# Kernel optimization log

Hardware: AMD Instinct MI355X
Metric: run time of the kernel (lower is better)

Reference implementation:

```python
import jax, jax.numpy as jnp
import numpy as np

NEG = -1000000.0  # mask value used by the torch module


def setup_inputs() -> dict:
    key = jax.random.key(0)
    kq, kk, kv, kl = jax.random.split(key, 4)
    B, Lq, Lk, d = 16, 2048, 2048, 128
    queries = jax.random.normal(kq, (B, Lq, d), dtype=jnp.float32)
    keys = jax.random.normal(kk, (B, Lk, d), dtype=jnp.float32)
    values = jax.random.normal(kv, (B, Lk, d), dtype=jnp.float32)
    valid_lens = jax.random.randint(kl, (B,), 1, Lk + 1, dtype=jnp.int64)
    return {"queries": queries, "keys": keys, "values": values, "valid_lens": valid_lens}


def reference(queries, keys, values, valid_lens):
    d = queries.shape[-1]
    # scores: [B, Lq, Lk]
    scores = jnp.einsum("bqd,bkd->bqk", queries, keys) / jnp.sqrt(jnp.asarray(d, queries.dtype))
    # valid_lens is [B]; mask key positions >= valid_len (broadcast over query rows)
    Lk = keys.shape[1]
    mask = jnp.arange(Lk)[None, None, :] < valid_lens[:, None, None]  # [B, 1, Lk]
    scores = jnp.where(mask, scores, NEG)
    attn = jax.nn.softmax(scores, axis=-1)
    # dropout p=0.0 -> identity
    return jnp.einsum("bqk,bkd->bqd", attn, values)
```

## Files before the change

kernel.cpp:

```cpp
#include <hip/hip_runtime.h>
#include <hip/hip_fp16.h>


typedef _Float16 f16x2 __attribute__((ext_vector_type(2)));
typedef _Float16 f16x8 __attribute__((ext_vector_type(8)));
typedef __fp16   n16x2 __attribute__((ext_vector_type(2)));
typedef float    f32x4 __attribute__((ext_vector_type(4)));
typedef float    f32x16 __attribute__((ext_vector_type(16)));
typedef unsigned int  u32;
typedef unsigned int  u32x4 __attribute__((ext_vector_type(4)));

#define LQ 2048
#define LK 2048
#define DIM 128
#define TILEB 16384
#define HTILEB 8192
#define BATCHB (32 * TILEB)
#define CFIX 10.0f

__device__ __forceinline__ f16x2 cvt2(float a, float b) {
    n16x2 t = __builtin_amdgcn_cvt_pkrtz(a, b);
    return __builtin_bit_cast(f16x2, t);
}
__device__ __forceinline__ u32 cvt2u(float a, float b) {
    return __builtin_bit_cast(u32, __builtin_amdgcn_cvt_pkrtz(a, b));
}

__device__ __forceinline__ f16x8 pk8(float4 a, float4 b) {
    f16x2 p0 = cvt2(a.x, a.y), p1 = cvt2(a.z, a.w);
    f16x2 p2 = cvt2(b.x, b.y), p3 = cvt2(b.z, b.w);
    f16x8 r;
    r[0]=p0[0]; r[1]=p0[1]; r[2]=p1[0]; r[3]=p1[1];
    r[4]=p2[0]; r[5]=p2[1]; r[6]=p3[0]; r[7]=p3[1];
    return r;
}

__global__ __launch_bounds__(256)
void prepK_kernel(const float* __restrict__ K, char* __restrict__ Kf,
                  const int* __restrict__ VLg) {
    size_t e = ((size_t)blockIdx.x * 256 + threadIdx.x) * 8;
    size_t krow = e >> 7; int d0 = (int)(e & 127);
    size_t b = krow >> 11; int k = (int)(krow & 2047);
    if (k >= VLg[b]) return;
    float4 a = *(const float4*)(K + e);
    float4 c = *(const float4*)(K + e + 4);
    int t = k >> 6, g = (k >> 5) & 1, lo = k & 31;
    int u = d0 >> 3, dc = u >> 1, hi = u & 1;
    char* out = Kf + ((b * 32 + t) * 16 + g * 8 + dc) * 1024 + (hi * 32 + lo) * 16;
    *(f16x8*)out = pk8(a, c);
}

__global__ __launch_bounds__(256)
void prepV_kernel(const float* __restrict__ V, char* __restrict__ Vf,
                  const int* __restrict__ VLg) {
    __shared__ _Float16 tl[64 * 136];
    const int blk = blockIdx.x, tid = threadIdx.x;
    const int b = blk >> 5, t = blk & 31, k0g = t * 64;
    if (k0g >= VLg[b]) return;
    const float* src = V + ((size_t)b * LK + k0g) * DIM;
    #pragma unroll
    for (int i = 0; i < 4; ++i) {
        int e = i * 2048 + tid * 8;
        int row = e >> 7, d = e & 127;
        float4 a = *(const float4*)(src + row * DIM + d);
        float4 c = *(const float4*)(src + row * DIM + d + 4);
        *(f16x8*)(&tl[row * 136 + d]) = pk8(a, c);
    }
    __syncthreads();
    char* out = Vf + (size_t)(b * 32 + t) * TILEB;
    #pragma unroll
    for (int c = 0; c < 4; ++c) {
        int chunk = tid * 4 + c;
        int f2 = chunk >> 6, l = chunk & 63;
        int ks = f2 >> 2, dc2 = f2 & 3;
        int k0 = ks * 16 + (l >> 5) * 8;
        int d  = dc2 * 32 + (l & 31);
        f16x8 w;
        #pragma unroll
        for (int j = 0; j < 8; ++j) w[j] = tl[(k0 + j) * 136 + d];
        *(f16x8*)(out + f2 * 1024 + l * 16) = w;
    }
}

__global__ __launch_bounds__(256, 2)
void fa_kernel(const float* __restrict__ Qg, const char* __restrict__ Kf,
               const char* __restrict__ Vf, const int* __restrict__ VLg,
               float* __restrict__ Og)
{
    __shared__ float scr_o[2][32 * 128];
    __shared__ float scr_l[2][32];

    const int tid = threadIdx.x, wv = tid >> 6, lane = tid & 63;
    const int lo = lane & 31, hi = lane >> 5;
    const int qh = wv & 1, kh = wv >> 1;
    const int blk = blockIdx.x;

    unsigned long long ord = 0;
    {
        int vl[16];
        #pragma unroll
        for (int i = 0; i < 16; ++i) vl[i] = VLg[i];
        unsigned used = 0;
        #pragma unroll
        for (int r = 0; r < 16; ++r) {
            int best = 0, bl = -1;
            #pragma unroll
            for (int i = 0; i < 16; ++i)
                if (!((used >> i) & 1) && vl[i] > bl) { bl = vl[i]; best = i; }
            used |= 1u << best;
            ord |= (unsigned long long)best << (4 * r);
        }
    }
    const int half = blk >> 8, slot = blk & 15, j = (blk >> 4) & 15;
    const int rank = half ? (15 - slot) : slot;
    const int b    = (int)((ord >> (4 * rank)) & 15);
    const int qt   = half ? (16 + j) : j;
    const int q0   = qt * 64 + qh * 32;

    const int nvalid = VLg[b];
    const int H = (nvalid + 31) >> 5;
    const float SCL = 0.08838834764831845f * 1.44269504088896341f;

    const char* Kfb = Kf + (size_t)b * BATCHB + lane * 16;
    const char* Vfb = Vf + (size_t)b * BATCHB + lane * 16;

    f16x8 qf[8];
    {
        const float* qr = Qg + ((size_t)b*LQ + q0 + lo)*DIM + hi*8;
        #pragma unroll
        for (int dc = 0; dc < 8; ++dc) {
            float4 a = *(const float4*)(qr + dc*16);
            float4 c = *(const float4*)(qr + dc*16 + 4);
            a.x*=SCL; a.y*=SCL; a.z*=SCL; a.w*=SCL;
            c.x*=SCL; c.y*=SCL; c.z*=SCL; c.w*=SCL;
            qf[dc] = pk8(a, c);
        }
    }

    f32x16 oacc[4];
    #pragma unroll
    for (int d = 0; d < 4; ++d)
        #pragma unroll
        for (int r = 0; r < 16; ++r) oacc[d][r] = 0.f;
    float lrow = 0.f;

    f16x8 kA[8], kB[8], vC[8];

    auto load_k = [&](f16x8* kf, int h) {
        const char* kp = Kfb + (size_t)h * HTILEB;
        #pragma unroll
        for (int f = 0; f < 8; ++f) kf[f] = *(const f16x8*)(kp + f * 1024);
    };
    auto load_v = [&](int h) {
        const char* vp = Vfb + (size_t)h * HTILEB;
        #pragma unroll
        for (int f = 0; f < 8; ++f) vC[f] = *(const f16x8*)(vp + f * 1024);
    };

    auto compute = [&](const f16x8* kf, int h) {
        f32x16 s;
        #pragma unroll
        for (int r = 0; r < 16; ++r) s[r] = 0.f;
        __builtin_amdgcn_s_setprio(1);
        #pragma unroll
        for (int dc = 0; dc < 8; ++dc)
            s = __builtin_amdgcn_mfma_f32_32x32x16_f16(kf[dc], qf[dc], s, 0, 0, 0);
        __builtin_amdgcn_s_setprio(0);

        if ((h + 1) * 32 > nvalid) {
            const int k0 = h * 32;
            #pragma unroll
            for (int r = 0; r < 16; ++r) {
                int key = k0 + (r & 3) + 8 * (r >> 2) + 4 * hi;
                if (key >= nvalid) s[r] = -1e30f;
            }
        }

        u32 c[8];
        float rs = 0.f;
        #pragma unroll
        for (int m = 0; m < 8; ++m) {
            float a0 = __builtin_amdgcn_exp2f(s[2*m]   - CFIX);
            float a1 = __builtin_amdgcn_exp2f(s[2*m+1] - CFIX);
            rs += a0 + a1;
            c[m] = cvt2u(a0, a1);
        }
        lrow += rs;

        u32 w[8];
        #pragma unroll
        for (int m = 0; m < 8; ++m) w[m] = __shfl_xor(c[m], 32);
        f16x8 pa0 = __builtin_bit_cast(f16x8, hi ? (u32x4){w[2],w[3],c[2],c[3]}
                                                 : (u32x4){c[0],c[1],w[0],w[1]});
        f16x8 pa1 = __builtin_bit_cast(f16x8, hi ? (u32x4){w[6],w[7],c[6],c[7]}
                                                 : (u32x4){c[4],c[5],w[4],w[5]});

        __builtin_amdgcn_s_setprio(1);
        #pragma unroll
        for (int dc2 = 0; dc2 < 4; ++dc2) {
            oacc[dc2] = __builtin_amdgcn_mfma_f32_32x32x16_f16(pa0, vC[    dc2], oacc[dc2], 0,0,0);
            oacc[dc2] = __builtin_amdgcn_mfma_f32_32x32x16_f16(pa1, vC[4 + dc2], oacc[dc2], 0,0,0);
        }
        __builtin_amdgcn_s_setprio(0);
    };

    int h = kh;
    if (h < H) load_k(kA, h);
    while (h < H) {
        const int h2 = h + 2, h4 = h + 4;
        load_v(h);
        if (h2 < H) load_k(kB, h2);
        compute(kA, h);
        if (h2 < H) {
            load_v(h2);
            if (h4 < H) load_k(kA, h4);
            compute(kB, h2);
        }
        h = h4;
    }

    lrow += __shfl_xor(lrow, 32);

    if (kh == 1) {
        float* so = &scr_o[qh][0];
        #pragma unroll
        for (int r = 0; r < 16; ++r) {
            int qr = (r & 3) + 8 * (r >> 2) + 4 * hi;
            #pragma unroll
            for (int dc2 = 0; dc2 < 4; ++dc2)
                so[qr * 128 + dc2 * 32 + lo] = oacc[dc2][r];
        }
        if (hi == 0) scr_l[qh][lo] = lrow;
    }
    __syncthreads();
    if (kh == 0) {
        const float* so = &scr_o[qh][0];
        float lt = lrow + scr_l[qh][lo];
        float linv = 1.f / lt;
        #pragma unroll
        for (int r = 0; r < 16; ++r) {
            int qr = (r & 3) + 8 * (r >> 2) + 4 * hi;
            float lv = __shfl(linv, qr);
            float* orow = Og + ((size_t)b*LQ + q0 + qr)*DIM + lo;
            #pragma unroll
            for (int dc2 = 0; dc2 < 4; ++dc2)
                orow[dc2*32] = (oacc[dc2][r] + so[qr * 128 + dc2 * 32 + lo]) * lv;
        }
    }
}

typedef _Float16 f16x4_t __attribute__((ext_vector_type(4)));
__device__ __forceinline__ float fel(const float4& a, const float4& b, int d) {
    const float arr[8] = {a.x,a.y,a.z,a.w,b.x,b.y,b.z,b.w};
    return arr[d];
}
__device__ __forceinline__ int kfo(int r, int dbyte) {
    return ((r << 8) + dbyte) ^ ((r & 7) << 4);
}
__device__ __forceinline__ int vto(int d, int k) {
    return d*128 + ((((k >> 3) ^ ((d ^ (d >> 3)) & 7)) << 4) + (k & 7) * 2);
}

__global__ __launch_bounds__(256, 2)
void fa_fb(const float* __restrict__ Qg, const float* __restrict__ Kg,
           const float* __restrict__ Vg, const int* __restrict__ VLg,
           float* __restrict__ Og)
{
    __shared__ __align__(16) char ldsbuf[2][32768];
    __shared__ __align__(16) char ldsP[4][2048];
    const int tid = threadIdx.x, wv = tid >> 6, lane = tid & 63;
    const int lg = lane >> 4, ln = lane & 15;
    const int blk = blockIdx.x;
    const int b = 2 * (blk & 7) + ((blk >> 3) & 1);
    const int q0 = (blk >> 4) * 64 + wv * 16;
    const int nvalid = VLg[b];
    const int nt = (nvalid + 63) >> 6;
    const float SCL = 0.08838834764831845f * 1.44269504088896341f;
    const float* Kb32 = Kg + (size_t)b * LK * DIM;
    const float* Vb32 = Vg + (size_t)b * LK * DIM;
    float4 ka[4], kb4[4], va[4], vb[4];
    auto issue = [&](int t) {
        int k0 = t * 64;
        #pragma unroll
        for (int i = 0; i < 4; ++i) {
            int c = tid + i*256, row = c >> 4, d0 = (c & 15) * 8;
            const float* s = Kb32 + (size_t)(k0 + row)*DIM + d0;
            ka[i] = *(const float4*)s;  kb4[i] = *(const float4*)(s+4);
        }
        int kq = tid >> 4, d0 = (tid & 15) * 8;
        #pragma unroll
        for (int j = 0; j < 4; ++j) {
            const float* s = Vb32 + (size_t)(k0 + kq*4 + j)*DIM + d0;
            va[j] = *(const float4*)s;  vb[j] = *(const float4*)(s+4);
        }
    };
    auto swr = [&](int buf) {
        char* kb = &ldsbuf[buf][0];
        char* vb2 = &ldsbuf[buf][16384];
        #pragma unroll
        for (int i = 0; i < 4; ++i) {
            int c = tid + i*256, row = c >> 4, d0 = (c & 15) * 8;
            *(f16x8*)(kb + kfo(row, d0 << 1)) = pk8(ka[i], kb4[i]);
        }
        int kq = tid >> 4, d0 = (tid & 15) * 8;
        #pragma unroll
        for (int dd = 0; dd < 8; ++dd) {
            f16x2 lw = cvt2(fel(va[0],vb[0],dd), fel(va[1],vb[1],dd));
            f16x2 hw = cvt2(fel(va[2],vb[2],dd), fel(va[3],vb[3],dd));
            f16x4_t w; w[0]=lw[0]; w[1]=lw[1]; w[2]=hw[0]; w[3]=hw[1];
            *(f16x4_t*)(vb2 + vto(d0 + dd, 4*kq)) = w;
        }
    };
    issue(0);
    f16x8 qf[4];
    {
        const float* qr = Qg + ((size_t)b*LQ + q0 + ln)*DIM + lg*8;
        #pragma unroll
        for (int dc = 0; dc < 4; ++dc) {
            float4 a = *(const float4*)(qr + dc*32);
            float4 c = *(const float4*)(qr + dc*32 + 4);
            a.x*=SCL; a.y*=SCL; a.z*=SCL; a.w*=SCL;
            c.x*=SCL; c.y*=SCL; c.z*=SCL; c.w*=SCL;
            qf[dc] = pk8(a, c);
        }
    }
    swr(0);
    __syncthreads();
    f32x4 acc[8];
    #pragma unroll
    for (int t = 0; t < 8; ++t) acc[t] = (f32x4){0.f,0.f,0.f,0.f};
    float lrow = 0.f;
    char* pbase = &ldsP[wv][0];
    int cur = 0;
    for (int t = 0; t < nt; ++t) {
        const int k0 = t * 64;
        const bool more = (t + 1 < nt);
        if (more) issue(t + 1);
        char* kbase = &ldsbuf[cur][0];
        char* vbase = &ldsbuf[cur][16384];
        f32x4 s[4];
        #pragma unroll
        for (int kc = 0; kc < 4; ++kc) s[kc] = (f32x4){0.f,0.f,0.f,0.f};
        #pragma unroll
        for (int kc = 0; kc < 4; ++kc)
            #pragma unroll
            for (int dc = 0; dc < 4; ++dc) {
                f16x8 kf = *(const f16x8*)(kbase + kfo(kc*16 + ln, dc*64 + lg*16));
                s[kc] = __builtin_amdgcn_mfma_f32_16x16x32_f16(kf, qf[dc], s[kc], 0,0,0);
            }
        if (k0 + 64 > nvalid) {
            #pragma unroll
            for (int kc = 0; kc < 4; ++kc)
                #pragma unroll
                for (int r = 0; r < 4; ++r)
                    if (k0 + kc*16 + 4*lg + r >= nvalid) s[kc][r] = -1e30f;
        }
        float rs = 0.f;
        #pragma unroll
        for (int kc = 0; kc < 4; ++kc) {
            float p0 = __builtin_amdgcn_exp2f(s[kc][0] - CFIX);
            float p1 = __builtin_amdgcn_exp2f(s[kc][1] - CFIX);
            float p2 = __builtin_amdgcn_exp2f(s[kc][2] - CFIX);
            float p3 = __builtin_amdgcn_exp2f(s[kc][3] - CFIX);
            rs += (p0 + p1) + (p2 + p3);
            f16x2 plo = cvt2(p0, p1);
            f16x2 phi = cvt2(p2, p3);
            f16x4_t w; w[0]=plo[0]; w[1]=plo[1]; w[2]=phi[0]; w[3]=phi[1];
            *(f16x4_t*)(pbase + (ln << 7) + ((kc*32 + lg*8) ^ ((ln & 7) << 4))) = w;
        }
        lrow += rs;
        asm volatile("s_waitcnt lgkmcnt(0)" ::: "memory");
        f16x8 af[2];
        #pragma unroll
        for (int kc2 = 0; kc2 < 2; ++kc2)
            af[kc2] = *(const f16x8*)(pbase + (ln << 7) + ((kc2*64 + lg*16) ^ ((ln & 7) << 4)));
        #pragma unroll
        for (int tt = 0; tt < 8; ++tt)
            #pragma unroll
            for (int kc2 = 0; kc2 < 2; ++kc2) {
                f16x8 bf = *(const f16x8*)(vbase + vto(tt*16 + ln, kc2*32 + lg*8));
                acc[tt] = __builtin_amdgcn_mfma_f32_16x16x32_f16(af[kc2], bf, acc[tt], 0,0,0);
            }
        if (more) { swr(cur ^ 1); __syncthreads(); cur ^= 1; }
    }
    lrow += __shfl_xor(lrow, 16);
    lrow += __shfl_xor(lrow, 32);
    float linv = 1.f / lrow;
    #pragma unroll
    for (int r = 0; r < 4; ++r) {
        float lr = __shfl(linv, 4*lg + r);
        float* orow = Og + ((size_t)b*LQ + q0 + 4*lg + r)*DIM + ln;
        #pragma unroll
        for (int tt = 0; tt < 8; ++tt) orow[tt*16] = acc[tt][r] * lr;
    }
}

extern "C" void kernel_launch(void* const* d_in, const int* in_sizes, int n_in,
                              void* d_out, int out_size, void* d_ws, size_t ws_size,
                              hipStream_t stream) {
    const float* Q  = (const float*)d_in[0];
    const float* K  = (const float*)d_in[1];
    const float* V  = (const float*)d_in[2];
    const int*   VL = (const int*)d_in[3];
    float* O = (float*)d_out;

    const size_t need = (size_t)16 * BATCHB * 2;
    if (ws_size >= need) {
        char* Kf = (char*)d_ws;
        char* Vf = Kf + (size_t)16 * BATCHB;
        prepK_kernel<<<dim3(2048), dim3(256), 0, stream>>>(K, Kf, VL);
        prepV_kernel<<<dim3(512),  dim3(256), 0, stream>>>(V, Vf, VL);
        fa_kernel<<<dim3(512), dim3(256), 0, stream>>>(Q, Kf, Vf, VL, O);
    } else {
        fa_fb<<<dim3(512), dim3(256), 0, stream>>>(Q, K, V, VL, O);
    }
}
```

Measured before the change: 53.83 us.

## Stage K/V tiles through double-buffered LDS via global_load_lds shared across waves

```diff
diff --git a/kernel.cpp b/kernel.cpp
--- a/kernel.cpp
+++ b/kernel.cpp
@@ -87,8 +87,7 @@
                const char* __restrict__ Vf, const int* __restrict__ VLg,
                float* __restrict__ Og)
 {
-    __shared__ float scr_o[2][32 * 128];
-    __shared__ float scr_l[2][32];
+    __shared__ __align__(16) char ldsbuf[2][2][16384];
 
     const int tid = threadIdx.x, wv = tid >> 6, lane = tid & 63;
     const int lo = lane & 31, hi = lane >> 5;
@@ -119,10 +118,11 @@
 
     const int nvalid = VLg[b];
     const int H = (nvalid + 31) >> 5;
+    const int T = (H + 1) >> 1;
     const float SCL = 0.08838834764831845f * 1.44269504088896341f;
 
-    const char* Kfb = Kf + (size_t)b * BATCHB + lane * 16;
-    const char* Vfb = Vf + (size_t)b * BATCHB + lane * 16;
+    const char* Kfb = Kf + (size_t)b * BATCHB;
+    const char* Vfb = Vf + (size_t)b * BATCHB;
 
     f16x8 qf[8];
     {
@@ -144,27 +144,30 @@
         for (int r = 0; r < 16; ++r) oacc[d][r] = 0.f;
     float lrow = 0.f;
 
-    f16x8 kA[8], kB[8], vC[8];
-
-    auto load_k = [&](f16x8* kf, int h) {
-        const char* kp = Kfb + (size_t)h * HTILEB;
-        #pragma unroll
-        for (int f = 0; f < 8; ++f) kf[f] = *(const f16x8*)(kp + f * 1024);
+    auto dma = [&](int bu, int h) {
+        const char* src = (qh ? Vfb : Kfb) + (size_t)h * HTILEB + lane * 16;
+        char* dst = &ldsbuf[kh][bu][qh ? 8192 : 0];
+        #pragma unroll
+        for (int c = 0; c < 8; ++c)
+            __builtin_amdgcn_global_load_lds(
+                (const __attribute__((address_space(1))) unsigned*)(src + c * 1024),
+                (__attribute__((address_space(3))) unsigned*)(dst + c * 1024),
+                16, 0, 0);
     };
-    auto load_v = [&](int h) {
-        const char* vp = Vfb + (size_t)h * HTILEB;
-        #pragma unroll
-        for (int f = 0; f < 8; ++f) vC[f] = *(const f16x8*)(vp + f * 1024);
-    };
-
-    auto compute = [&](const f16x8* kf, int h) {
+
+    auto compute = [&](int cur, int h) {
+        char* ldsK = &ldsbuf[kh][cur][0];
+        char* ldsV = &ldsbuf[kh][cur][8192];
+
         f32x16 s;
         #pragma unroll
         for (int r = 0; r < 16; ++r) s[r] = 0.f;
         __builtin_amdgcn_s_setprio(1);
         #pragma unroll
-        for (int dc = 0; dc < 8; ++dc)
-            s = __builtin_amdgcn_mfma_f32_32x32x16_f16(kf[dc], qf[dc], s, 0, 0, 0);
+        for (int dc = 0; dc < 8; ++dc) {
+            f16x8 kfr = *(const f16x8*)(ldsK + dc * 1024 + lane * 16);
+            s = __builtin_amdgcn_mfma_f32_32x32x16_f16(kfr, qf[dc], s, 0, 0, 0);
+        }
         __builtin_amdgcn_s_setprio(0);
 
         if ((h + 1) * 32 > nvalid) {
@@ -198,44 +201,43 @@
         __builtin_amdgcn_s_setprio(1);
         #pragma unroll
         for (int dc2 = 0; dc2 < 4; ++dc2) {
-            oacc[dc2] = __builtin_amdgcn_mfma_f32_32x32x16_f16(pa0, vC[    dc2], oacc[dc2], 0,0,0);
-            oacc[dc2] = __builtin_amdgcn_mfma_f32_32x32x16_f16(pa1, vC[4 + dc2], oacc[dc2], 0,0,0);
+            f16x8 v0 = *(const f16x8*)(ldsV + (    dc2) * 1024 + lane * 16);
+            f16x8 v1 = *(const f16x8*)(ldsV + (4 + dc2) * 1024 + lane * 16);
+            oacc[dc2] = __builtin_amdgcn_mfma_f32_32x32x16_f16(pa0, v0, oacc[dc2], 0,0,0);
+            oacc[dc2] = __builtin_amdgcn_mfma_f32_32x32x16_f16(pa1, v1, oacc[dc2], 0,0,0);
         }
         __builtin_amdgcn_s_setprio(0);
     };
 
-    int h = kh;
-    if (h < H) load_k(kA, h);
-    while (h < H) {
-        const int h2 = h + 2, h4 = h + 4;
-        load_v(h);
-        if (h2 < H) load_k(kB, h2);
-        compute(kA, h);
-        if (h2 < H) {
-            load_v(h2);
-            if (h4 < H) load_k(kA, h4);
-            compute(kB, h2);
-        }
-        h = h4;
+    int cur = 0;
+    if (kh < H) dma(0, kh);
+    __syncthreads();
+    for (int it = 0; it < T; ++it) {
+        const int h  = kh + 2 * it;
+        const int hn = h + 2;
+        if (hn < H) dma(cur ^ 1, hn);
+        if (h < H) compute(cur, h);
+        __syncthreads();
+        cur ^= 1;
     }
 
     lrow += __shfl_xor(lrow, 32);
 
+    float* scr_o = (float*)&ldsbuf[0][0][0] + qh * 4096;
+    float* scr_l = (float*)&ldsbuf[1][0][0];
     if (kh == 1) {
-        float* so = &scr_o[qh][0];
         #pragma unroll
         for (int r = 0; r < 16; ++r) {
             int qr = (r & 3) + 8 * (r >> 2) + 4 * hi;
             #pragma unroll
             for (int dc2 = 0; dc2 < 4; ++dc2)
-                so[qr * 128 + dc2 * 32 + lo] = oacc[dc2][r];
-        }
-        if (hi == 0) scr_l[qh][lo] = lrow;
+                scr_o[qr * 128 + dc2 * 32 + lo] = oacc[dc2][r];
+        }
+        if (hi == 0) scr_l[qh * 32 + lo] = lrow;
     }
     __syncthreads();
     if (kh == 0) {
-        const float* so = &scr_o[qh][0];
-        float lt = lrow + scr_l[qh][lo];
+        float lt = lrow + scr_l[qh * 32 + lo];
         float linv = 1.f / lt;
         #pragma unroll
         for (int r = 0; r < 16; ++r) {
@@ -244,7 +246,7 @@
             float* orow = Og + ((size_t)b*LQ + q0 + qr)*DIM + lo;
             #pragma unroll
             for (int dc2 = 0; dc2 < 4; ++dc2)
-                orow[dc2*32] = (oacc[dc2][r] + so[qr * 128 + dc2 * 32 + lo]) * lv;
+                orow[dc2*32] = (oacc[dc2][r] + scr_o[qr * 128 + dc2 * 32 + lo]) * lv;
         }
     }
 }
```

Measured after the change: 60.06 us. 11.6% more time.
